# Kernel tuning notes

Hardware: AMD Instinct MI355X
Metric: run time of the kernel (lower is better)

## Reference

```python
import jax, jax.numpy as jnp
import numpy as np

T, B, I, H, O = 512, 128, 512, 512, 12

def setup_inputs() -> dict:
    key = jax.random.key(0)
    ks = jax.random.split(key, 17)
    def w(k, shape):
        # xavier-normal-ish init
        std = float(np.sqrt(2.0 / (shape[0] + shape[-1])))
        return jax.random.normal(k, shape, dtype=jnp.float32) * std
    return {
        "x": jax.random.normal(ks[0], (T, B, I), dtype=jnp.float32),
        "w0": w(ks[1], (O, H)), "wz": w(ks[2], (O, H)), "wr": w(ks[3], (O, H)),
        "ws": w(ks[4], (I, H)),
        "wa": w(ks[5], (H, H)), "ua": w(ks[6], (I, H)), "va": w(ks[7], (H, 1)),
        "u0": w(ks[8], (H, H)), "uz": w(ks[9], (H, H)), "ur": w(ks[10], (H, H)),
        "c0": w(ks[11], (I, H)), "cz": w(ks[12], (I, H)), "cr": w(ks[13], (I, H)),
        "fc_w": w(ks[14], (H, O)),
        "fc_b": jnp.zeros((O,), dtype=jnp.float32),
        "max_labels": 16,
    }

def reference(x, w0, wz, wr, ws, wa, ua, va, u0, uz, ur, c0, cz, cr, fc_w, fc_b, max_labels):
    # x: [T, B, I] encoder states; decode max_labels steps of a Bahdanau-attention GRU.
    s0 = jnp.tanh(x[0] @ ws)              # [B, H]
    out0 = s0 @ fc_w + fc_b               # [B, O]
    U = jnp.einsum('tbi,ih->tbh', x, ua)  # precomputed encoder projection
    va_v = va[:, 0]                       # [H]

    def step(carry, _):
        s, out = carry                                          # [B,H], [B,O]
        e = jnp.einsum('tbh,h->tb', jnp.tanh(s @ wa + U), va_v)  # [T,B] additive scores
        a = jax.nn.softmax(e, axis=0)                           # attention over T
        c = jnp.einsum('tb,tbi->bi', a, x)                      # [B,I] context
        r = jax.nn.sigmoid(out @ wr + s @ ur + c @ cr)
        z = jax.nn.sigmoid(out @ wz + s @ uz + c @ cz)
        sh = jnp.tanh(out @ w0 + (r * s) @ u0 + c @ c0)
        s_new = (1.0 - z) * s + z * sh
        out_new = s_new @ fc_w + fc_b
        return (s_new, out_new), out_new

    _, outs = jax.lax.scan(step, (s0, out0), None, length=max_labels - 1)
    all_outs = jnp.concatenate([out0[None], outs], axis=0)  # [L, B, O]
    return jnp.transpose(all_outs, (1, 0, 2))               # [B, L, O]
```

## Files before the change

### kernel.cpp

```cpp
#include <hip/hip_runtime.h>

#define NSTEP 16

typedef __attribute__((ext_vector_type(8))) short s16x8;
typedef __attribute__((ext_vector_type(4))) float f32x4;
typedef __attribute__((ext_vector_type(2))) float f32x2;

__device__ __forceinline__ float bf2f(unsigned short u){
  union { unsigned int i; float f; } v; v.i = ((unsigned int)u) << 16; return v.f;
}
__device__ __forceinline__ unsigned short f2bf(float f){
  union { float f; unsigned int i; } v; v.f = f;
  unsigned int r = v.i + 0x7fffu + ((v.i >> 16) & 1u);
  return (unsigned short)(r >> 16);
}
__device__ __forceinline__ unsigned char f2fp8(float f){
  return (unsigned char)(__builtin_amdgcn_cvt_pk_fp8_f32(f, f, 0, false) & 0xff);
}
__device__ __forceinline__ float fast_rcp(float x){ return __builtin_amdgcn_rcpf(x); }
__device__ __forceinline__ float fast_tanh(float x){
  float e = __expf(2.0f * x);
  return 1.0f - 2.0f * fast_rcp(e + 1.0f);
}
__device__ __forceinline__ float fast_sigmoid(float x){
  return fast_rcp(1.0f + __expf(-x));
}
__device__ __forceinline__ void gload16(const void* g, void* l){
  __builtin_amdgcn_global_load_lds((const __attribute__((address_space(1))) void*)g,
                                   (__attribute__((address_space(3))) void*)l, 16, 0, 0);
}
__device__ __forceinline__ float wave_sum(float v){
#pragma unroll
  for (int off = 32; off; off >>= 1) v += __shfl_xor(v, off, 64);
  return v;
}
__device__ __forceinline__ float wave_max(float v){
#pragma unroll
  for (int off = 32; off; off >>= 1) v = fmaxf(v, __shfl_xor(v, off, 64));
  return v;
}
__device__ __forceinline__ void fp8x8_dec(uint2 w, float* u){
  f32x2 d0 = __builtin_amdgcn_cvt_pk_f32_fp8(w.x, false);
  f32x2 d1 = __builtin_amdgcn_cvt_pk_f32_fp8(w.x, true);
  f32x2 d2 = __builtin_amdgcn_cvt_pk_f32_fp8(w.y, false);
  f32x2 d3 = __builtin_amdgcn_cvt_pk_f32_fp8(w.y, true);
  u[0] = d0[0]; u[1] = d0[1]; u[2] = d1[0]; u[3] = d1[1];
  u[4] = d2[0]; u[5] = d2[1]; u[6] = d3[0]; u[7] = d3[1];
}

struct GemmLDS { unsigned short A[64 * 64]; unsigned short B[128 * 64]; };

__global__ __launch_bounds__(512) void ugemm_k(
    const unsigned short* __restrict__ A, const unsigned short* __restrict__ Bt,
    unsigned char* __restrict__ o8){
  __shared__ GemmLDS lds;
  const int tid = threadIdx.x;
  const int lane = tid & 63, wid = tid >> 6;
  const int wr = wid >> 2, wc = wid & 3;
  const int mt = blockIdx.y, nt = blockIdx.x;
  f32x4 acc[2][2];
#pragma unroll
  for (int m = 0; m < 2; ++m)
#pragma unroll
    for (int n = 0; n < 2; ++n) acc[m][n] = (f32x4)0.0f;

  for (int kt = 0; kt < 512; kt += 64){
    __syncthreads();
    {
      int row = tid >> 3, kc = (tid & 7) ^ (row & 7);
      gload16(A + (size_t)(mt * 64 + row) * 512 + kt + kc * 8, &lds.A[tid * 8]);
#pragma unroll
      for (int p = 0; p < 2; ++p){
        int s = p * 512 + tid;
        int br = s >> 3, bkc = (s & 7) ^ (br & 7);
        gload16(Bt + (size_t)(nt * 128 + br) * 512 + kt + bkc * 8, &lds.B[s * 8]);
      }
    }
    __syncthreads();
#pragma unroll
    for (int ks = 0; ks < 2; ++ks){
      int kc_l = (lane >> 4) + ks * 4;
      s16x8 av[2], bv[2];
#pragma unroll
      for (int m = 0; m < 2; ++m){
        int r = wr * 32 + m * 16 + (lane & 15);
        av[m] = *(const s16x8*)&lds.A[r * 64 + ((kc_l ^ (r & 7)) << 3)];
      }
#pragma unroll
      for (int n = 0; n < 2; ++n){
        int c = wc * 32 + n * 16 + (lane & 15);
        bv[n] = *(const s16x8*)&lds.B[c * 64 + ((kc_l ^ (c & 7)) << 3)];
      }
#pragma unroll
      for (int m = 0; m < 2; ++m)
#pragma unroll
        for (int n = 0; n < 2; ++n)
          acc[m][n] = __builtin_amdgcn_mfma_f32_16x16x32_bf16(av[m], bv[n], acc[m][n], 0, 0, 0);
    }
  }
#pragma unroll
  for (int m = 0; m < 2; ++m)
#pragma unroll
    for (int n = 0; n < 2; ++n){
      int r_base = mt * 64 + wr * 32 + m * 16 + ((lane >> 4) << 2);
      int col = nt * 128 + wc * 32 + n * 16 + (lane & 15);
#pragma unroll
      for (int q = 0; q < 4; ++q)
        o8[(size_t)(r_base + q) * 512 + col] = f2fp8(acc[m][n][q]);
    }
}

struct FLDS { unsigned short A[64 * 256]; unsigned short B[64 * 256]; };

template<int EPI>
__device__ __forceinline__ void fgemm_body(int mt, int nt,
    const unsigned short* __restrict__ A, const unsigned short* __restrict__ Bt,
    unsigned short* __restrict__ ob0, float* __restrict__ o0, float* __restrict__ o1,
    const float* __restrict__ e0, const float* __restrict__ e1,
    const float* __restrict__ e2, const float* __restrict__ e3,
    FLDS& lds){
  const int tid = threadIdx.x;
  const int lane = tid & 63, wid = tid >> 6;
  const int wr = wid >> 1, wc = wid & 1;
  f32x4 acc[2];
  acc[0] = (f32x4)0.0f; acc[1] = (f32x4)0.0f;

  for (int kt = 0; kt < 512; kt += 256){
    if (kt) __syncthreads();
#pragma unroll
    for (int i = 0; i < 4; ++i){
      int s = i * 512 + tid;
      int row = s >> 5, c = s & 31;
      int sc = (c & 24) | ((c & 7) ^ (row & 7));
      gload16(A + (size_t)(mt * 64 + row) * 512 + kt + sc * 8, &lds.A[s * 8]);
      gload16(Bt + (size_t)(nt * 64 + row) * 512 + kt + sc * 8, &lds.B[s * 8]);
    }
    __syncthreads();
#pragma unroll
    for (int kk = 0; kk < 8; ++kk){
      int kch = kk * 4 + (lane >> 4);
      int ar = wr * 16 + (lane & 15);
      int asw = (kch & 24) | ((kch & 7) ^ (ar & 7));
      s16x8 av = *(const s16x8*)&lds.A[ar * 256 + asw * 8];
#pragma unroll
      for (int n = 0; n < 2; ++n){
        int br = wc * 32 + n * 16 + (lane & 15);
        int bsw = (kch & 24) | ((kch & 7) ^ (br & 7));
        s16x8 bv = *(const s16x8*)&lds.B[br * 256 + bsw * 8];
        acc[n] = __builtin_amdgcn_mfma_f32_16x16x32_bf16(av, bv, acc[n], 0, 0, 0);
      }
    }
  }

#pragma unroll
  for (int n = 0; n < 2; ++n){
    int r_base = mt * 64 + wr * 16 + ((lane >> 4) << 2);
    int col = nt * 64 + wc * 32 + n * 16 + (lane & 15);
#pragma unroll
    for (int q = 0; q < 4; ++q){
      float v = acc[n][q];
      size_t r_ = (size_t)(r_base + q);
      if constexpr (EPI == 1){
        float t = fast_tanh(v);
        o0[r_ * 512 + col] = t;
        ob0[r_ * 512 + col] = f2bf(t);
      } else if constexpr (EPI == 2){
        o0[r_ * 1536 + col] = v;
      } else if constexpr (EPI == 3){
        float op = 0.f;
        const float* wo = e1 + (size_t)col * 12;
        const float* ob = e0 + r_ * 12;
#pragma unroll
        for (int o = 0; o < 12; ++o) op += ob[o] * wo[o];
        float v2 = v + op;
        if (col < 1024) v2 += e3[r_ * 1536 + 512 + col];
        if (col < 512){
          float rg = fast_sigmoid(v2);
          ob0[r_ * 512 + col] = f2bf(rg * e2[r_ * 512 + col]);
        } else if (col < 1024){
          o0[r_ * 512 + (col - 512)] = fast_sigmoid(v2);
        } else {
          o1[r_ * 512 + (col - 1024)] = v2;
        }
      } else if constexpr (EPI == 4){
        float v2 = v + e0[r_ * 512 + col];
        float sh = fast_tanh(v2);
        float z  = e1[r_ * 512 + col];
        float so = o0[r_ * 512 + col];
        float sn = (1.0f - z) * so + z * sh;
        o0[r_ * 512 + col] = sn;
        ob0[r_ * 512 + col] = f2bf(sn);
      }
    }
  }
}

template<int EPI>
__global__ __launch_bounds__(512) void fgemm_k(
    const unsigned short* __restrict__ A, const unsigned short* __restrict__ Bt,
    unsigned short* __restrict__ ob0, float* __restrict__ o0, float* __restrict__ o1,
    const float* __restrict__ e0, const float* __restrict__ e1,
    const float* __restrict__ e2, const float* __restrict__ e3){
  __shared__ FLDS lds;
  fgemm_body<EPI>(blockIdx.y, blockIdx.x, A, Bt, ob0, o0, o1, e0, e1, e2, e3, lds);
}

__device__ __forceinline__ void out_fc_b(int b, int lane, int step,
    const float* __restrict__ s_f32, const float* __restrict__ fcwT,
    const float* __restrict__ fcb, float* __restrict__ outb, float* __restrict__ dout){
  const float* sp = s_f32 + (size_t)b * 512 + lane * 8;
  float4 sa = *(const float4*)sp, sb = *(const float4*)(sp + 4);
#pragma unroll
  for (int o = 0; o < 12; ++o){
    const float* fp = fcwT + (size_t)o * 512 + lane * 8;
    float4 fa = *(const float4*)fp, fb = *(const float4*)(fp + 4);
    float sum = sa.x * fa.x + sa.y * fa.y + sa.z * fa.z + sa.w * fa.w +
                sb.x * fb.x + sb.y * fb.y + sb.z * fb.z + sb.w * fb.w;
    sum = wave_sum(sum);
    if (lane == 0){
      float v = sum + fcb[o];
      outb[b * 12 + o] = v;
      dout[(size_t)b * (NSTEP * 12) + step * 12 + o] = v;
    }
  }
}

__global__ __launch_bounds__(512) void step1_k(
    const unsigned short* __restrict__ s_bf, const unsigned short* __restrict__ P1w,
    float* __restrict__ pre1, const float* __restrict__ s_f32,
    const float* __restrict__ fcwT, const float* __restrict__ fcb,
    float* __restrict__ outb, float* __restrict__ dout, int prev_step){
  __shared__ FLDS lds;
  int bid = blockIdx.x;
  if (bid < 48){
    fgemm_body<2>(bid / 24, bid % 24, s_bf, P1w, nullptr, pre1, nullptr,
                  nullptr, nullptr, nullptr, nullptr, lds);
  } else {
    int lane = threadIdx.x & 63, wid = threadIdx.x >> 6;
    out_fc_b((bid - 48) * 8 + wid, lane, prev_step, s_f32, fcwT, fcb, outb, dout);
  }
}

__global__ __launch_bounds__(256) void e_k(const unsigned char* __restrict__ U8,
    const float* __restrict__ pre1, const float* __restrict__ va,
    float* __restrict__ e_bt){
  int b = blockIdx.y, tc = blockIdx.x;
  int lane = threadIdx.x & 63, wid = threadIdx.x >> 6;
  const float* pp = pre1 + (size_t)b * 1536 + lane * 8;
  float4 s0v = *(const float4*)pp, s1v = *(const float4*)(pp + 4);
  const float* vp = va + lane * 8;
  float4 v0 = *(const float4*)vp, v1 = *(const float4*)(vp + 4);
  float sv[8] = {s0v.x, s0v.y, s0v.z, s0v.w, s1v.x, s1v.y, s1v.z, s1v.w};
  float vv[8] = {v0.x, v0.y, v0.z, v0.w, v1.x, v1.y, v1.z, v1.w};
  int t0 = tc * 64 + wid * 16;
#pragma unroll 4
  for (int i = 0; i < 16; ++i){
    int t = t0 + i;
    uint2 w = *(const uint2*)(U8 + ((size_t)t * 128 + b) * 512 + lane * 8);
    float u[8];
    fp8x8_dec(w, u);
    float sum = 0.f;
#pragma unroll
    for (int k = 0; k < 8; ++k)
      sum += fast_tanh(u[k] + sv[k]) * vv[k];
    sum = wave_sum(sum);
    if (lane == 0) e_bt[(size_t)b * 512 + t] = sum;
  }
}

__global__ __launch_bounds__(256) void c_k(const unsigned char* __restrict__ x8,
    const float* __restrict__ e_bt, unsigned short* __restrict__ cbf){
  __shared__ float a_s[512];
  __shared__ float red[8];
  __shared__ float cred[4][128];
  int b = blockIdx.y, ic = blockIdx.x;
  int tid = threadIdx.x;
  int lane = tid & 63, wid = tid >> 6;
  float e0v = e_bt[(size_t)b * 512 + tid];
  float e1v = e_bt[(size_t)b * 512 + 256 + tid];
  float m = wave_max(fmaxf(e0v, e1v));
  if (lane == 0) red[wid] = m;
  __syncthreads();
  m = fmaxf(fmaxf(red[0], red[1]), fmaxf(red[2], red[3]));
  float p0 = __expf(e0v - m), p1 = __expf(e1v - m);
  float s = wave_sum(p0 + p1);
  if (lane == 0) red[4 + wid] = s;
  __syncthreads();
  float den = red[4] + red[5] + red[6] + red[7];
  float rden = fast_rcp(den);
  a_s[tid] = p0 * rden;
  a_s[tid + 256] = p1 * rden;
  __syncthreads();
  int lane16 = lane & 15, q4 = lane >> 4;
  float acc[8] = {0, 0, 0, 0, 0, 0, 0, 0};
  for (int round = 0; round < 32; ++round){
    int t = round * 16 + wid * 4 + q4;
    float a = a_s[t];
    uint2 w = *(const uint2*)(x8 + ((size_t)t * 128 + b) * 512 + ic * 128 + lane16 * 8);
    float u[8];
    fp8x8_dec(w, u);
#pragma unroll
    for (int k = 0; k < 8; ++k) acc[k] += a * u[k];
  }
#pragma unroll
  for (int k = 0; k < 8; ++k){
    acc[k] += __shfl_xor(acc[k], 16, 64);
    acc[k] += __shfl_xor(acc[k], 32, 64);
  }
  if (q4 == 0){
#pragma unroll
    for (int k = 0; k < 8; ++k) cred[wid][lane16 * 8 + k] = acc[k];
  }
  __syncthreads();
  if (tid < 128){
    float cs = cred[0][tid] + cred[1][tid] + cred[2][tid] + cred[3][tid];
    cbf[(size_t)b * 512 + ic * 128 + tid] = f2bf(cs);
  }
}

__global__ __launch_bounds__(512) void outtail_k(const float* __restrict__ s_f32,
    const float* __restrict__ fcwT, const float* __restrict__ fcb,
    float* __restrict__ outb, float* __restrict__ dout){
  int lane = threadIdx.x & 63, wid = threadIdx.x >> 6;
  out_fc_b(blockIdx.x * 8 + wid, lane, NSTEP - 1, s_f32, fcwT, fcb, outb, dout);
}

__global__ __launch_bounds__(256) void castx_k(const float* __restrict__ x,
    unsigned short* __restrict__ xb, unsigned char* __restrict__ x8){
  size_t idx = (size_t)blockIdx.x * 256 + threadIdx.x;
  const float* p = x + idx * 8;
  float4 a = *(const float4*)p, b = *(const float4*)(p + 4);
  s16x8 t8;
  t8[0] = (short)f2bf(a.x); t8[1] = (short)f2bf(a.y);
  t8[2] = (short)f2bf(a.z); t8[3] = (short)f2bf(a.w);
  t8[4] = (short)f2bf(b.x); t8[5] = (short)f2bf(b.y);
  t8[6] = (short)f2bf(b.z); t8[7] = (short)f2bf(b.w);
  *(s16x8*)(xb + idx * 8) = t8;
  unsigned int lo, hi;
  lo = __builtin_amdgcn_cvt_pk_fp8_f32(a.x, a.y, 0, false);
  lo = __builtin_amdgcn_cvt_pk_fp8_f32(a.z, a.w, lo, true);
  hi = __builtin_amdgcn_cvt_pk_fp8_f32(b.x, b.y, 0, false);
  hi = __builtin_amdgcn_cvt_pk_fp8_f32(b.z, b.w, hi, true);
  uint2 w; w.x = lo; w.y = hi;
  *(uint2*)(x8 + idx * 8) = w;
}

__global__ __launch_bounds__(512) void trans_k(
    const float* __restrict__ ua, const float* __restrict__ wsm,
    const float* __restrict__ wa, const float* __restrict__ urm,
    const float* __restrict__ uz, const float* __restrict__ cr,
    const float* __restrict__ cz, const float* __restrict__ c0,
    const float* __restrict__ u0, const float* __restrict__ wrm,
    const float* __restrict__ wzm, const float* __restrict__ w0m,
    const float* __restrict__ fcw,
    unsigned short* __restrict__ Pua, unsigned short* __restrict__ Pws,
    unsigned short* __restrict__ P1w, unsigned short* __restrict__ P2w,
    unsigned short* __restrict__ P3w, float* __restrict__ Wo2,
    float* __restrict__ fcwT){
  __shared__ unsigned short tr[64][72];
  int bid = blockIdx.x, tid = threadIdx.x;
  if (bid < 576){
    int mi = bid >> 6, tile = bid & 63;
    int trr = tile >> 3, tcc = tile & 7;
    const float* src; unsigned short* dst;
    switch (mi){
      case 0: src = ua;  dst = Pua;              break;
      case 1: src = wsm; dst = Pws;              break;
      case 2: src = wa;  dst = P1w;              break;
      case 3: src = urm; dst = P1w + 512 * 512;  break;
      case 4: src = uz;  dst = P1w + 1024 * 512; break;
      case 5: src = cr;  dst = P2w;              break;
      case 6: src = cz;  dst = P2w + 512 * 512;  break;
      case 7: src = c0;  dst = P2w + 1024 * 512; break;
      default:src = u0;  dst = P3w;              break;
    }
    int r = tid >> 3, c8 = (tid & 7) * 8;
    const float* sp = src + (size_t)(trr * 64 + r) * 512 + tcc * 64 + c8;
    float4 a = *(const float4*)sp, b = *(const float4*)(sp + 4);
    unsigned short* lp = &tr[r][c8];
    lp[0] = f2bf(a.x); lp[1] = f2bf(a.y); lp[2] = f2bf(a.z); lp[3] = f2bf(a.w);
    lp[4] = f2bf(b.x); lp[5] = f2bf(b.y); lp[6] = f2bf(b.z); lp[7] = f2bf(b.w);
    __syncthreads();
    s16x8 o8v;
#pragma unroll
    for (int k = 0; k < 8; ++k) o8v[k] = (short)tr[c8 + k][r];
    *(s16x8*)(dst + (size_t)(tcc * 64 + r) * 512 + trr * 64 + c8) = o8v;
  } else {
    int gidx = (bid - 576) * 512 + tid;
    if (gidx < 18432){
      int p = gidx / 6144, e = gidx % 6144;
      int o = e >> 9, h = e & 511;
      const float* w_ = (p == 0) ? wrm : (p == 1) ? wzm : w0m;
      Wo2[(size_t)(p * 512 + h) * 12 + o] = w_[o * 512 + h];
    } else if (gidx < 24576){
      int e = gidx - 18432;
      int h = e / 12, o = e - h * 12;
      fcwT[(size_t)o * 512 + h] = fcw[h * 12 + o];
    }
  }
}

extern "C" void kernel_launch(void* const* d_in, const int* in_sizes, int n_in,
                              void* d_out, int out_size, void* d_ws, size_t ws_size,
                              hipStream_t stream){
  const float* x   = (const float*)d_in[0];
  const float* w0  = (const float*)d_in[1];
  const float* wz  = (const float*)d_in[2];
  const float* wrm = (const float*)d_in[3];
  const float* wsm = (const float*)d_in[4];
  const float* wa  = (const float*)d_in[5];
  const float* ua  = (const float*)d_in[6];
  const float* va  = (const float*)d_in[7];
  const float* u0  = (const float*)d_in[8];
  const float* uz  = (const float*)d_in[9];
  const float* urm = (const float*)d_in[10];
  const float* c0  = (const float*)d_in[11];
  const float* cz  = (const float*)d_in[12];
  const float* cr  = (const float*)d_in[13];
  const float* fcw = (const float*)d_in[14];
  const float* fcb = (const float*)d_in[15];
  float* dout = (float*)d_out;

  char* base = (char*)d_ws;
  size_t off = 0;
  auto alloc = [&](size_t bytes) -> char* {
    char* p = base + off; off += (bytes + 255) & ~(size_t)255; return p;
  };
  unsigned short* xb   = (unsigned short*)alloc((size_t)512 * 128 * 512 * 2);
  unsigned char*  x8   = (unsigned char*) alloc((size_t)512 * 128 * 512);
  unsigned char*  U8   = (unsigned char*) alloc((size_t)512 * 128 * 512);
  unsigned short* Pua  = (unsigned short*)alloc(512 * 512 * 2);
  unsigned short* Pws  = (unsigned short*)alloc(512 * 512 * 2);
  unsigned short* P1w  = (unsigned short*)alloc((size_t)1536 * 512 * 2);
  unsigned short* P2w  = (unsigned short*)alloc((size_t)1536 * 512 * 2);
  unsigned short* P3w  = (unsigned short*)alloc(512 * 512 * 2);
  float* Wo2           = (float*)alloc(1536 * 12 * 4);
  float* fcwT          = (float*)alloc(12 * 512 * 4);
  float* pre1          = (float*)alloc((size_t)128 * 1536 * 4);
  float* e_bt          = (float*)alloc((size_t)128 * 512 * 4);
  unsigned short* cbf  = (unsigned short*)alloc((size_t)128 * 512 * 2);
  unsigned short* rsb  = (unsigned short*)alloc((size_t)128 * 512 * 2);
  float* zbuf          = (float*)alloc((size_t)128 * 512 * 4);
  float* cu0           = (float*)alloc((size_t)128 * 512 * 4);
  float* s_f32         = (float*)alloc((size_t)128 * 512 * 4);
  unsigned short* s_bf = (unsigned short*)alloc((size_t)128 * 512 * 2);
  float* outb          = (float*)alloc(128 * 12 * 4);
  (void)ws_size; (void)in_sizes; (void)n_in; (void)out_size;

  castx_k<<<16384, 256, 0, stream>>>(x, xb, x8);
  trans_k<<<624, 512, 0, stream>>>(ua, wsm, wa, urm, uz, cr, cz, c0, u0,
                                   wrm, wz, w0, fcw,
                                   Pua, Pws, P1w, P2w, P3w, Wo2, fcwT);
  ugemm_k<<<dim3(4, 1024), 512, 0, stream>>>(xb, Pua, U8);
  fgemm_k<1><<<dim3(8, 2), 512, 0, stream>>>(xb, Pws, s_bf, s_f32, nullptr,
                                             nullptr, nullptr, nullptr, nullptr);

  for (int step = 1; step < NSTEP; ++step){
    step1_k<<<64, 512, 0, stream>>>(s_bf, P1w, pre1, s_f32, fcwT, fcb,
                                    outb, dout, step - 1);
    e_k<<<dim3(8, 128), 256, 0, stream>>>(U8, pre1, va, e_bt);
    c_k<<<dim3(4, 128), 256, 0, stream>>>(x8, e_bt, cbf);
    fgemm_k<3><<<dim3(24, 2), 512, 0, stream>>>(cbf, P2w, rsb, zbuf, cu0,
                                                outb, Wo2, s_f32, pre1);
    fgemm_k<4><<<dim3(8, 2), 512, 0, stream>>>(rsb, P3w, s_bf, s_f32, nullptr,
                                               cu0, zbuf, nullptr, nullptr);
  }
  outtail_k<<<16, 512, 0, stream>>>(s_f32, fcwT, fcb, outb, dout);
}
```

Measured before the change: 806.0 us.

## Fold output projection into recurrent weights and fuse attention score with context

Uses the identity out = s@fc_w + fc_b to precompute fc_w@W_{r,z,0} into an extended s-projection weight plus a bias. This removes the per-step output matmul and the Wo2 epilogue. The separate score and softmax-context kernels become one ec_k that exponentiates scores without max subtraction and accumulates split-T partial contexts. gates_k normalizes and sums those partials while staging its A tile. States are kept in a history buffer so all outputs come from one final kernel, which cuts per-step launches. Skipping the max subtraction relies on scores staying bounded and adds some overflow risk.

```diff
diff --git a/kernel.cpp b/kernel.cpp
--- a/kernel.cpp
+++ b/kernel.cpp
@@ -32,11 +32,6 @@
 __device__ __forceinline__ float wave_sum(float v){
 #pragma unroll
   for (int off = 32; off; off >>= 1) v += __shfl_xor(v, off, 64);
-  return v;
-}
-__device__ __forceinline__ float wave_max(float v){
-#pragma unroll
-  for (int off = 32; off; off >>= 1) v = fmaxf(v, __shfl_xor(v, off, 64));
   return v;
 }
 __device__ __forceinline__ void fp8x8_dec(uint2 w, float* u){
@@ -115,10 +110,9 @@
 template<int EPI>
 __device__ __forceinline__ void fgemm_body(int mt, int nt,
     const unsigned short* __restrict__ A, const unsigned short* __restrict__ Bt,
-    unsigned short* __restrict__ ob0, float* __restrict__ o0, float* __restrict__ o1,
+    unsigned short* __restrict__ ob0, float* __restrict__ o0,
     const float* __restrict__ e0, const float* __restrict__ e1,
-    const float* __restrict__ e2, const float* __restrict__ e3,
-    FLDS& lds){
+    const float* __restrict__ e2, FLDS& lds){
   const int tid = threadIdx.x;
   const int lane = tid & 63, wid = tid >> 6;
   const int wr = wid >> 1, wc = wid & 1;
@@ -165,28 +159,12 @@
         o0[r_ * 512 + col] = t;
         ob0[r_ * 512 + col] = f2bf(t);
       } else if constexpr (EPI == 2){
-        o0[r_ * 1536 + col] = v;
-      } else if constexpr (EPI == 3){
-        float op = 0.f;
-        const float* wo = e1 + (size_t)col * 12;
-        const float* ob = e0 + r_ * 12;
-#pragma unroll
-        for (int o = 0; o < 12; ++o) op += ob[o] * wo[o];
-        float v2 = v + op;
-        if (col < 1024) v2 += e3[r_ * 1536 + 512 + col];
-        if (col < 512){
-          float rg = fast_sigmoid(v2);
-          ob0[r_ * 512 + col] = f2bf(rg * e2[r_ * 512 + col]);
-        } else if (col < 1024){
-          o0[r_ * 512 + (col - 512)] = fast_sigmoid(v2);
-        } else {
-          o1[r_ * 512 + (col - 1024)] = v2;
-        }
+        o0[r_ * 2048 + col] = v + e0[col];
       } else if constexpr (EPI == 4){
         float v2 = v + e0[r_ * 512 + col];
         float sh = fast_tanh(v2);
         float z  = e1[r_ * 512 + col];
-        float so = o0[r_ * 512 + col];
+        float so = e2[r_ * 512 + col];
         float sn = (1.0f - z) * so + z * sh;
         o0[r_ * 512 + col] = sn;
         ob0[r_ * 512 + col] = f2bf(sn);
@@ -198,17 +176,147 @@
 template<int EPI>
 __global__ __launch_bounds__(512) void fgemm_k(
     const unsigned short* __restrict__ A, const unsigned short* __restrict__ Bt,
-    unsigned short* __restrict__ ob0, float* __restrict__ o0, float* __restrict__ o1,
+    unsigned short* __restrict__ ob0, float* __restrict__ o0,
     const float* __restrict__ e0, const float* __restrict__ e1,
-    const float* __restrict__ e2, const float* __restrict__ e3){
+    const float* __restrict__ e2){
   __shared__ FLDS lds;
-  fgemm_body<EPI>(blockIdx.y, blockIdx.x, A, Bt, ob0, o0, o1, e0, e1, e2, e3, lds);
-}
-
-__device__ __forceinline__ void out_fc_b(int b, int lane, int step,
-    const float* __restrict__ s_f32, const float* __restrict__ fcwT,
-    const float* __restrict__ fcb, float* __restrict__ outb, float* __restrict__ dout){
-  const float* sp = s_f32 + (size_t)b * 512 + lane * 8;
+  fgemm_body<EPI>(blockIdx.y, blockIdx.x, A, Bt, ob0, o0, e0, e1, e2, lds);
+}
+
+__global__ __launch_bounds__(512) void ec_k(const unsigned char* __restrict__ U8,
+    const unsigned char* __restrict__ x8, const float* __restrict__ pre1,
+    const float* __restrict__ va, float* __restrict__ cpart, float* __restrict__ psum){
+  __shared__ float cred[8][512];
+  __shared__ float pred[8];
+  int chunk = blockIdx.x, b = blockIdx.y;
+  int tid = threadIdx.x, lane = tid & 63, wid = tid >> 6;
+  const float* pp = pre1 + (size_t)b * 2048 + lane * 8;
+  float4 p0 = *(const float4*)pp, p1 = *(const float4*)(pp + 4);
+  const float* vp = va + lane * 8;
+  float4 v0 = *(const float4*)vp, v1 = *(const float4*)(vp + 4);
+  float sv[8] = {p0.x, p0.y, p0.z, p0.w, p1.x, p1.y, p1.z, p1.w};
+  float vv[8] = {v0.x, v0.y, v0.z, v0.w, v1.x, v1.y, v1.z, v1.w};
+  float acc[8] = {0, 0, 0, 0, 0, 0, 0, 0};
+  float psum_l = 0.f;
+  int t0 = chunk * 256 + wid * 32;
+  for (int i = 0; i < 32; ++i){
+    int t = t0 + i;
+    uint2 w = *(const uint2*)(U8 + ((size_t)t * 128 + b) * 512 + lane * 8);
+    float u[8];
+    fp8x8_dec(w, u);
+    float e = 0.f;
+#pragma unroll
+    for (int k = 0; k < 8; ++k)
+      e += fast_tanh(u[k] + sv[k]) * vv[k];
+    e = wave_sum(e);
+    float p = __expf(e);
+    psum_l += p;
+    uint2 wx = *(const uint2*)(x8 + ((size_t)t * 128 + b) * 512 + lane * 8);
+    float ux[8];
+    fp8x8_dec(wx, ux);
+#pragma unroll
+    for (int k = 0; k < 8; ++k) acc[k] += p * ux[k];
+  }
+#pragma unroll
+  for (int k = 0; k < 8; ++k) cred[wid][lane * 8 + k] = acc[k];
+  if (lane == 0) pred[wid] = psum_l;
+  __syncthreads();
+  float cs = 0.f;
+#pragma unroll
+  for (int w = 0; w < 8; ++w) cs += cred[w][tid];
+  cpart[((size_t)chunk * 128 + b) * 512 + tid] = cs;
+  if (tid == 0){
+    float s = 0.f;
+#pragma unroll
+    for (int w = 0; w < 8; ++w) s += pred[w];
+    psum[chunk * 128 + b] = s;
+  }
+}
+
+__global__ __launch_bounds__(512) void gates_k(
+    const float* __restrict__ cpart, const float* __restrict__ psum,
+    const unsigned short* __restrict__ P2w, const float* __restrict__ pre1,
+    const float* __restrict__ s_prev,
+    unsigned short* __restrict__ rsb, float* __restrict__ zbuf, float* __restrict__ cu0){
+  __shared__ FLDS lds;
+  __shared__ float rden_s[64];
+  const int tid = threadIdx.x;
+  const int lane = tid & 63, wid = tid >> 6;
+  const int wr = wid >> 1, wc = wid & 1;
+  const int nt = blockIdx.x, mt = blockIdx.y;
+  if (tid < 64){
+    float d = psum[mt * 64 + tid] + psum[128 + mt * 64 + tid];
+    rden_s[tid] = fast_rcp(d);
+  }
+  f32x4 acc[2];
+  acc[0] = (f32x4)0.0f; acc[1] = (f32x4)0.0f;
+
+  for (int kt = 0; kt < 512; kt += 256){
+    __syncthreads();
+#pragma unroll
+    for (int i = 0; i < 4; ++i){
+      int s = i * 512 + tid;
+      int row = s >> 5, c = s & 31;
+      int sc = (c & 24) | ((c & 7) ^ (row & 7));
+      int b = mt * 64 + row;
+      const float* cp0 = cpart + (size_t)b * 512 + kt + sc * 8;
+      const float* cp1 = cp0 + (size_t)128 * 512;
+      float rd = rden_s[row];
+      float4 a0 = *(const float4*)cp0, a1 = *(const float4*)(cp0 + 4);
+      float4 b0 = *(const float4*)cp1, b1 = *(const float4*)(cp1 + 4);
+      s16x8 t8;
+      t8[0] = (short)f2bf((a0.x + b0.x) * rd); t8[1] = (short)f2bf((a0.y + b0.y) * rd);
+      t8[2] = (short)f2bf((a0.z + b0.z) * rd); t8[3] = (short)f2bf((a0.w + b0.w) * rd);
+      t8[4] = (short)f2bf((a1.x + b1.x) * rd); t8[5] = (short)f2bf((a1.y + b1.y) * rd);
+      t8[6] = (short)f2bf((a1.z + b1.z) * rd); t8[7] = (short)f2bf((a1.w + b1.w) * rd);
+      *(s16x8*)&lds.A[s * 8] = t8;
+      gload16(P2w + (size_t)(nt * 64 + row) * 512 + kt + sc * 8, &lds.B[s * 8]);
+    }
+    __syncthreads();
+#pragma unroll
+    for (int kk = 0; kk < 8; ++kk){
+      int kch = kk * 4 + (lane >> 4);
+      int ar = wr * 16 + (lane & 15);
+      int asw = (kch & 24) | ((kch & 7) ^ (ar & 7));
+      s16x8 av = *(const s16x8*)&lds.A[ar * 256 + asw * 8];
+#pragma unroll
+      for (int n = 0; n < 2; ++n){
+        int br = wc * 32 + n * 16 + (lane & 15);
+        int bsw = (kch & 24) | ((kch & 7) ^ (br & 7));
+        s16x8 bv = *(const s16x8*)&lds.B[br * 256 + bsw * 8];
+        acc[n] = __builtin_amdgcn_mfma_f32_16x16x32_bf16(av, bv, acc[n], 0, 0, 0);
+      }
+    }
+  }
+
+#pragma unroll
+  for (int n = 0; n < 2; ++n){
+    int r_base = mt * 64 + wr * 16 + ((lane >> 4) << 2);
+    int col = nt * 64 + wc * 32 + n * 16 + (lane & 15);
+#pragma unroll
+    for (int q = 0; q < 4; ++q){
+      float v = acc[n][q];
+      size_t r_ = (size_t)(r_base + q);
+      float v2 = v + pre1[r_ * 2048 + 512 + col];
+      if (col < 512){
+        float rg = fast_sigmoid(v2);
+        rsb[r_ * 512 + col] = f2bf(rg * s_prev[r_ * 512 + col]);
+      } else if (col < 1024){
+        zbuf[r_ * 512 + (col - 512)] = fast_sigmoid(v2);
+      } else {
+        cu0[r_ * 512 + (col - 1024)] = v2;
+      }
+    }
+  }
+}
+
+__global__ __launch_bounds__(512) void dout_k(const float* __restrict__ s_hist,
+    const float* __restrict__ fcwT, const float* __restrict__ fcb,
+    float* __restrict__ dout){
+  int lane = threadIdx.x & 63, wid = threadIdx.x >> 6;
+  int w = blockIdx.x * 8 + wid;
+  int step = w >> 7, b = w & 127;
+  const float* sp = s_hist + (size_t)w * 512 + lane * 8;
   float4 sa = *(const float4*)sp, sb = *(const float4*)(sp + 4);
 #pragma unroll
   for (int o = 0; o < 12; ++o){
@@ -217,112 +325,9 @@
     float sum = sa.x * fa.x + sa.y * fa.y + sa.z * fa.z + sa.w * fa.w +
                 sb.x * fb.x + sb.y * fb.y + sb.z * fb.z + sb.w * fb.w;
     sum = wave_sum(sum);
-    if (lane == 0){
-      float v = sum + fcb[o];
-      outb[b * 12 + o] = v;
-      dout[(size_t)b * (NSTEP * 12) + step * 12 + o] = v;
-    }
-  }
-}
-
-__global__ __launch_bounds__(512) void step1_k(
-    const unsigned short* __restrict__ s_bf, const unsigned short* __restrict__ P1w,
-    float* __restrict__ pre1, const float* __restrict__ s_f32,
-    const float* __restrict__ fcwT, const float* __restrict__ fcb,
-    float* __restrict__ outb, float* __restrict__ dout, int prev_step){
-  __shared__ FLDS lds;
-  int bid = blockIdx.x;
-  if (bid < 48){
-    fgemm_body<2>(bid / 24, bid % 24, s_bf, P1w, nullptr, pre1, nullptr,
-                  nullptr, nullptr, nullptr, nullptr, lds);
-  } else {
-    int lane = threadIdx.x & 63, wid = threadIdx.x >> 6;
-    out_fc_b((bid - 48) * 8 + wid, lane, prev_step, s_f32, fcwT, fcb, outb, dout);
-  }
-}
-
-__global__ __launch_bounds__(256) void e_k(const unsigned char* __restrict__ U8,
-    const float* __restrict__ pre1, const float* __restrict__ va,
-    float* __restrict__ e_bt){
-  int b = blockIdx.y, tc = blockIdx.x;
-  int lane = threadIdx.x & 63, wid = threadIdx.x >> 6;
-  const float* pp = pre1 + (size_t)b * 1536 + lane * 8;
-  float4 s0v = *(const float4*)pp, s1v = *(const float4*)(pp + 4);
-  const float* vp = va + lane * 8;
-  float4 v0 = *(const float4*)vp, v1 = *(const float4*)(vp + 4);
-  float sv[8] = {s0v.x, s0v.y, s0v.z, s0v.w, s1v.x, s1v.y, s1v.z, s1v.w};
-  float vv[8] = {v0.x, v0.y, v0.z, v0.w, v1.x, v1.y, v1.z, v1.w};
-  int t0 = tc * 64 + wid * 16;
-#pragma unroll 4
-  for (int i = 0; i < 16; ++i){
-    int t = t0 + i;
-    uint2 w = *(const uint2*)(U8 + ((size_t)t * 128 + b) * 512 + lane * 8);
-    float u[8];
-    fp8x8_dec(w, u);
-    float sum = 0.f;
-#pragma unroll
-    for (int k = 0; k < 8; ++k)
-      sum += fast_tanh(u[k] + sv[k]) * vv[k];
-    sum = wave_sum(sum);
-    if (lane == 0) e_bt[(size_t)b * 512 + t] = sum;
-  }
-}
-
-__global__ __launch_bounds__(256) void c_k(const unsigned char* __restrict__ x8,
-    const float* __restrict__ e_bt, unsigned short* __restrict__ cbf){
-  __shared__ float a_s[512];
-  __shared__ float red[8];
-  __shared__ float cred[4][128];
-  int b = blockIdx.y, ic = blockIdx.x;
-  int tid = threadIdx.x;
-  int lane = tid & 63, wid = tid >> 6;
-  float e0v = e_bt[(size_t)b * 512 + tid];
-  float e1v = e_bt[(size_t)b * 512 + 256 + tid];
-  float m = wave_max(fmaxf(e0v, e1v));
-  if (lane == 0) red[wid] = m;
-  __syncthreads();
-  m = fmaxf(fmaxf(red[0], red[1]), fmaxf(red[2], red[3]));
-  float p0 = __expf(e0v - m), p1 = __expf(e1v - m);
-  float s = wave_sum(p0 + p1);
-  if (lane == 0) red[4 + wid] = s;
-  __syncthreads();
-  float den = red[4] + red[5] + red[6] + red[7];
-  float rden = fast_rcp(den);
-  a_s[tid] = p0 * rden;
-  a_s[tid + 256] = p1 * rden;
-  __syncthreads();
-  int lane16 = lane & 15, q4 = lane >> 4;
-  float acc[8] = {0, 0, 0, 0, 0, 0, 0, 0};
-  for (int round = 0; round < 32; ++round){
-    int t = round * 16 + wid * 4 + q4;
-    float a = a_s[t];
-    uint2 w = *(const uint2*)(x8 + ((size_t)t * 128 + b) * 512 + ic * 128 + lane16 * 8);
-    float u[8];
-    fp8x8_dec(w, u);
-#pragma unroll
-    for (int k = 0; k < 8; ++k) acc[k] += a * u[k];
-  }
-#pragma unroll
-  for (int k = 0; k < 8; ++k){
-    acc[k] += __shfl_xor(acc[k], 16, 64);
-    acc[k] += __shfl_xor(acc[k], 32, 64);
-  }
-  if (q4 == 0){
-#pragma unroll
-    for (int k = 0; k < 8; ++k) cred[wid][lane16 * 8 + k] = acc[k];
-  }
-  __syncthreads();
-  if (tid < 128){
-    float cs = cred[0][tid] + cred[1][tid] + cred[2][tid] + cred[3][tid];
-    cbf[(size_t)b * 512 + ic * 128 + tid] = f2bf(cs);
-  }
-}
-
-__global__ __launch_bounds__(512) void outtail_k(const float* __restrict__ s_f32,
-    const float* __restrict__ fcwT, const float* __restrict__ fcb,
-    float* __restrict__ outb, float* __restrict__ dout){
-  int lane = threadIdx.x & 63, wid = threadIdx.x >> 6;
-  out_fc_b(blockIdx.x * 8 + wid, lane, NSTEP - 1, s_f32, fcwT, fcb, outb, dout);
+    if (lane == 0)
+      dout[(size_t)b * (NSTEP * 12) + step * 12 + o] = sum + fcb[o];
+  }
 }
 
 __global__ __launch_bounds__(256) void castx_k(const float* __restrict__ x,
@@ -347,55 +352,82 @@
 
 __global__ __launch_bounds__(512) void trans_k(
     const float* __restrict__ ua, const float* __restrict__ wsm,
-    const float* __restrict__ wa, const float* __restrict__ urm,
-    const float* __restrict__ uz, const float* __restrict__ cr,
-    const float* __restrict__ cz, const float* __restrict__ c0,
-    const float* __restrict__ u0, const float* __restrict__ wrm,
+    const float* __restrict__ u0, const float* __restrict__ wa,
+    const float* __restrict__ urm, const float* __restrict__ uz,
+    const float* __restrict__ cr, const float* __restrict__ cz,
+    const float* __restrict__ c0, const float* __restrict__ wrm,
     const float* __restrict__ wzm, const float* __restrict__ w0m,
-    const float* __restrict__ fcw,
+    const float* __restrict__ fcw, const float* __restrict__ fcb,
     unsigned short* __restrict__ Pua, unsigned short* __restrict__ Pws,
-    unsigned short* __restrict__ P1w, unsigned short* __restrict__ P2w,
-    unsigned short* __restrict__ P3w, float* __restrict__ Wo2,
-    float* __restrict__ fcwT){
+    unsigned short* __restrict__ P3w, unsigned short* __restrict__ P1w,
+    unsigned short* __restrict__ P2w, float* __restrict__ fcwT,
+    float* __restrict__ bias_full){
   __shared__ unsigned short tr[64][72];
   int bid = blockIdx.x, tid = threadIdx.x;
-  if (bid < 576){
+  if (bid < 640){
     int mi = bid >> 6, tile = bid & 63;
     int trr = tile >> 3, tcc = tile & 7;
-    const float* src; unsigned short* dst;
+    const float* src = nullptr; const float* W = nullptr; unsigned short* dst;
     switch (mi){
-      case 0: src = ua;  dst = Pua;              break;
-      case 1: src = wsm; dst = Pws;              break;
-      case 2: src = wa;  dst = P1w;              break;
-      case 3: src = urm; dst = P1w + 512 * 512;  break;
-      case 4: src = uz;  dst = P1w + 1024 * 512; break;
-      case 5: src = cr;  dst = P2w;              break;
-      case 6: src = cz;  dst = P2w + 512 * 512;  break;
-      case 7: src = c0;  dst = P2w + 1024 * 512; break;
-      default:src = u0;  dst = P3w;              break;
+      case 0: src = ua;  dst = Pua;               break;
+      case 1: src = wsm; dst = Pws;               break;
+      case 2: src = u0;  dst = P3w;               break;
+      case 3: src = wa;  dst = P1w;               break;
+      case 4: src = urm; dst = P1w + 512 * 512;  W = wrm; break;
+      case 5: src = uz;  dst = P1w + 1024 * 512; W = wzm; break;
+      case 6: src = nullptr; dst = P1w + 1536 * 512; W = w0m; break;
+      case 7: src = cr;  dst = P2w;               break;
+      case 8: src = cz;  dst = P2w + 512 * 512;   break;
+      default:src = c0;  dst = P2w + 1024 * 512;  break;
     }
     int r = tid >> 3, c8 = (tid & 7) * 8;
-    const float* sp = src + (size_t)(trr * 64 + r) * 512 + tcc * 64 + c8;
-    float4 a = *(const float4*)sp, b = *(const float4*)(sp + 4);
+    int h = trr * 64 + r;
+    float vals[8];
+    if (src){
+      const float* sp = src + (size_t)h * 512 + tcc * 64 + c8;
+      float4 a = *(const float4*)sp, b = *(const float4*)(sp + 4);
+      vals[0] = a.x; vals[1] = a.y; vals[2] = a.z; vals[3] = a.w;
+      vals[4] = b.x; vals[5] = b.y; vals[6] = b.z; vals[7] = b.w;
+    } else {
+#pragma unroll
+      for (int k = 0; k < 8; ++k) vals[k] = 0.f;
+    }
+    if (W){
+      float fr[12];
+#pragma unroll
+      for (int o = 0; o < 12; ++o) fr[o] = fcw[h * 12 + o];
+#pragma unroll
+      for (int jj = 0; jj < 8; ++jj){
+        int j = tcc * 64 + c8 + jj;
+        float cj = 0.f;
+#pragma unroll
+        for (int o = 0; o < 12; ++o) cj += fr[o] * W[o * 512 + j];
+        vals[jj] += cj;
+      }
+    }
     unsigned short* lp = &tr[r][c8];
-    lp[0] = f2bf(a.x); lp[1] = f2bf(a.y); lp[2] = f2bf(a.z); lp[3] = f2bf(a.w);
-    lp[4] = f2bf(b.x); lp[5] = f2bf(b.y); lp[6] = f2bf(b.z); lp[7] = f2bf(b.w);
+#pragma unroll
+    for (int k = 0; k < 8; ++k) lp[k] = f2bf(vals[k]);
     __syncthreads();
     s16x8 o8v;
 #pragma unroll
     for (int k = 0; k < 8; ++k) o8v[k] = (short)tr[c8 + k][r];
     *(s16x8*)(dst + (size_t)(tcc * 64 + r) * 512 + trr * 64 + c8) = o8v;
+  } else if (bid < 652){
+    int gidx = (bid - 640) * 512 + tid;
+    int h = gidx / 12, o = gidx - h * 12;
+    fcwT[(size_t)o * 512 + h] = fcw[h * 12 + o];
   } else {
-    int gidx = (bid - 576) * 512 + tid;
-    if (gidx < 18432){
-      int p = gidx / 6144, e = gidx % 6144;
-      int o = e >> 9, h = e & 511;
-      const float* w_ = (p == 0) ? wrm : (p == 1) ? wzm : w0m;
-      Wo2[(size_t)(p * 512 + h) * 12 + o] = w_[o * 512 + h];
-    } else if (gidx < 24576){
-      int e = gidx - 18432;
-      int h = e / 12, o = e - h * 12;
-      fcwT[(size_t)o * 512 + h] = fcw[h * 12 + o];
+#pragma unroll
+    for (int p = 0; p < 4; ++p){
+      int col = p * 512 + tid;
+      float v = 0.f;
+      if (p > 0){
+        const float* W = (p == 1) ? wrm : (p == 2) ? wzm : w0m;
+#pragma unroll
+        for (int o = 0; o < 12; ++o) v += fcb[o] * W[o * 512 + tid];
+      }
+      bias_full[col] = v;
     }
   }
 }
@@ -431,39 +463,39 @@
   unsigned char*  U8   = (unsigned char*) alloc((size_t)512 * 128 * 512);
   unsigned short* Pua  = (unsigned short*)alloc(512 * 512 * 2);
   unsigned short* Pws  = (unsigned short*)alloc(512 * 512 * 2);
-  unsigned short* P1w  = (unsigned short*)alloc((size_t)1536 * 512 * 2);
+  unsigned short* P3w  = (unsigned short*)alloc(512 * 512 * 2);
+  unsigned short* P1w  = (unsigned short*)alloc((size_t)2048 * 512 * 2);
   unsigned short* P2w  = (unsigned short*)alloc((size_t)1536 * 512 * 2);
-  unsigned short* P3w  = (unsigned short*)alloc(512 * 512 * 2);
-  float* Wo2           = (float*)alloc(1536 * 12 * 4);
   float* fcwT          = (float*)alloc(12 * 512 * 4);
-  float* pre1          = (float*)alloc((size_t)128 * 1536 * 4);
-  float* e_bt          = (float*)alloc((size_t)128 * 512 * 4);
-  unsigned short* cbf  = (unsigned short*)alloc((size_t)128 * 512 * 2);
+  float* bias_full     = (float*)alloc(2048 * 4);
+  float* pre1          = (float*)alloc((size_t)128 * 2048 * 4);
+  float* cpart         = (float*)alloc((size_t)2 * 128 * 512 * 4);
+  float* psum          = (float*)alloc(2 * 128 * 4);
   unsigned short* rsb  = (unsigned short*)alloc((size_t)128 * 512 * 2);
   float* zbuf          = (float*)alloc((size_t)128 * 512 * 4);
   float* cu0           = (float*)alloc((size_t)128 * 512 * 4);
-  float* s_f32         = (float*)alloc((size_t)128 * 512 * 4);
+  float* s_hist        = (float*)alloc((size_t)NSTEP * 128 * 512 * 4);
   unsigned short* s_bf = (unsigned short*)alloc((size_t)128 * 512 * 2);
-  float* outb          = (float*)alloc(128 * 12 * 4);
   (void)ws_size; (void)in_sizes; (void)n_in; (void)out_size;
 
   castx_k<<<16384, 256, 0, stream>>>(x, xb, x8);
-  trans_k<<<624, 512, 0, stream>>>(ua, wsm, wa, urm, uz, cr, cz, c0, u0,
-                                   wrm, wz, w0, fcw,
-                                   Pua, Pws, P1w, P2w, P3w, Wo2, fcwT);
+  trans_k<<<653, 512, 0, stream>>>(ua, wsm, u0, wa, urm, uz, cr, cz, c0,
+                                   wrm, wz, w0, fcw, fcb,
+                                   Pua, Pws, P3w, P1w, P2w, fcwT, bias_full);
   ugemm_k<<<dim3(4, 1024), 512, 0, stream>>>(xb, Pua, U8);
-  fgemm_k<1><<<dim3(8, 2), 512, 0, stream>>>(xb, Pws, s_bf, s_f32, nullptr,
-                                             nullptr, nullptr, nullptr, nullptr);
+  fgemm_k<1><<<dim3(8, 2), 512, 0, stream>>>(xb, Pws, s_bf, s_hist,
+                                             nullptr, nullptr, nullptr);
 
   for (int step = 1; step < NSTEP; ++step){
-    step1_k<<<64, 512, 0, stream>>>(s_bf, P1w, pre1, s_f32, fcwT, fcb,
-                                    outb, dout, step - 1);
-    e_k<<<dim3(8, 128), 256, 0, stream>>>(U8, pre1, va, e_bt);
-    c_k<<<dim3(4, 128), 256, 0, stream>>>(x8, e_bt, cbf);
-    fgemm_k<3><<<dim3(24, 2), 512, 0, stream>>>(cbf, P2w, rsb, zbuf, cu0,
-                                                outb, Wo2, s_f32, pre1);
-    fgemm_k<4><<<dim3(8, 2), 512, 0, stream>>>(rsb, P3w, s_bf, s_f32, nullptr,
-                                               cu0, zbuf, nullptr, nullptr);
-  }
-  outtail_k<<<16, 512, 0, stream>>>(s_f32, fcwT, fcb, outb, dout);
-}
+    const float* s_prev = s_hist + (size_t)(step - 1) * 128 * 512;
+    float* s_cur = s_hist + (size_t)step * 128 * 512;
+    fgemm_k<2><<<dim3(32, 2), 512, 0, stream>>>(s_bf, P1w, nullptr, pre1,
+                                                bias_full, nullptr, nullptr);
+    ec_k<<<dim3(2, 128), 512, 0, stream>>>(U8, x8, pre1, va, cpart, psum);
+    gates_k<<<dim3(24, 2), 512, 0, stream>>>(cpart, psum, P2w, pre1, s_prev,
+                                             rsb, zbuf, cu0);
+    fgemm_k<4><<<dim3(8, 2), 512, 0, stream>>>(rsb, P3w, s_bf, s_cur,
+                                               cu0, zbuf, s_prev);
+  }
+  dout_k<<<256, 512, 0, stream>>>(s_hist, fcwT, fcb, dout);
+}
```

New measurement: 800.6 us. About the same (-0.7%).
